# Kernel tuning notes

Hardware: AMD Instinct MI355X
Metric: run time of the kernel (lower is better)

Reference implementation:

```python
import jax, jax.numpy as jnp
import numpy as np


def trident(w, thresholds, noise_sd, noise):
    # thresholded + noised ternarization to {-1, 0, +1}
    wn = w + noise_sd * noise
    return jnp.where(wn < thresholds[0], -1.0, jnp.where(wn > thresholds[1], 1.0, 0.0)).astype(w.dtype)


def setup_inputs() -> dict:
    key = jax.random.key(0)
    k1, k2, k3, k4 = jax.random.split(key, 4)
    B, in_features, num_experts, expert_size = 8192, 4096, 64, 128
    in_chunks = in_features // expert_size  # 32
    x = jax.random.normal(k1, (B, in_features), dtype=jnp.float32)
    # glorot-like scaling for params
    routing_matrix = jax.random.normal(k2, (in_chunks, num_experts), dtype=jnp.float32) * np.sqrt(2.0 / (in_chunks + num_experts))
    We = jax.random.normal(k3, (num_experts, expert_size, expert_size), dtype=jnp.float32) * np.sqrt(1.0 / expert_size)
    noise = jax.random.normal(k4, (in_chunks, num_experts), dtype=jnp.float32)
    return {"x": x, "routing_matrix": routing_matrix, "We": We, "noise": noise}


def reference(x, routing_matrix, We, noise):
    thresholds = (-0.5, 0.5)
    noise_sd = 0.1
    expert_size = We.shape[-1]
    B = x.shape[0]
    xc = x.reshape(B, -1, expert_size)                     # (B, in_chunks, d)
    ternary = trident(routing_matrix, thresholds, noise_sd, noise)  # (in_chunks, E)
    x_routed = jnp.einsum('ik,bij->bkj', ternary, xc)      # (B, E, d)
    x_experts = jnp.einsum('eij,bej->bei', We, x_routed)   # (B, E, d)
    return x_experts.reshape(B, -1)
```

## Files before the change

kernel.cpp:

```cpp
#include <hip/hip_runtime.h>

#define IC   32
#define NE   64
#define D    128
#define IF   4096
#define OF   8192
#define TB   128

__global__ __launch_bounds__(256, 1)
void trident_moe_kernel(const float* __restrict__ x,
                        const float* __restrict__ routing,
                        const float* __restrict__ We,
                        const float* __restrict__ noise,
                        float* __restrict__ out) {
    __shared__ float sWe[D * D];
    __shared__ float sXr[TB * D];
    __shared__ float s_sign[IC];
    __shared__ int   s_chunk[IC];
    __shared__ float s_csign[IC];
    __shared__ int   s_cnt;

    const int t  = threadIdx.x;
    const int e  = blockIdx.y;
    const int bt = blockIdx.x;

    if (t < IC) {
        float w  = routing[t * NE + e];
        float nz = noise[t * NE + e];
        float wn = __fadd_rn(w, __fmul_rn(0.1f, nz));
        s_sign[t] = (wn < -0.5f) ? -1.0f : ((wn > 0.5f) ? 1.0f : 0.0f);
    }
    __syncthreads();
    if (t == 0) {
        int c = 0;
        for (int i = 0; i < IC; ++i) {
            float s = s_sign[i];
            if (s != 0.0f) { s_chunk[c] = i; s_csign[c] = s; ++c; }
        }
        s_cnt = c;
    }
    __syncthreads();
    const int nnz = s_cnt;

    const int c4 = t & 31;
    const int r0 = t >> 5;

    float4* out4 = (float4*)out;
    const size_t orow4 = OF / 4;

    if (nnz == 0) {
        const float4 z = make_float4(0.f, 0.f, 0.f, 0.f);
        #pragma unroll
        for (int p = 0; p < TB / 8; ++p) {
            size_t row = (size_t)(bt * TB + p * 8 + r0);
            out4[row * orow4 + e * (D / 4) + c4] = z;
        }
        return;
    }

    const float4* We4 = (const float4*)(We + (size_t)e * D * D);
    #pragma unroll
    for (int p = 0; p < D / 8; ++p) {
        int r = p * 8 + r0;
        float4 w4 = We4[r * (D / 4) + c4];
        float wv[4] = {w4.x, w4.y, w4.z, w4.w};
        #pragma unroll
        for (int k = 0; k < 4; ++k) {
            int j = c4 * 4 + k;
            int blk = (r >> 3) ^ ((j >> 2) & 15);
            sWe[j * D + blk * 8 + (r & 7)] = wv[k];
        }
    }

    const float4* x4p = (const float4*)x;
    const size_t xrow4 = IF / 4;
    #pragma unroll
    for (int p = 0; p < TB / 8; ++p) {
        int b = p * 8 + r0;
        size_t row = (size_t)(bt * TB + b);
        float4 acc = make_float4(0.f, 0.f, 0.f, 0.f);
        for (int m = 0; m < nnz; ++m) {
            int   i = s_chunk[m];
            float s = s_csign[m];
            float4 v = x4p[row * xrow4 + i * (D / 4) + c4];
            acc.x += s * v.x; acc.y += s * v.y;
            acc.z += s * v.z; acc.w += s * v.w;
        }
        float av[4] = {acc.x, acc.y, acc.z, acc.w};
        #pragma unroll
        for (int k = 0; k < 4; ++k) {
            int j = c4 * 4 + k;
            int blk = (b >> 3) ^ ((j >> 2) & 15);
            sXr[j * TB + blk * 8 + (b & 7)] = av[k];
        }
    }
    __syncthreads();

    const int rg = t & 15;
    const int bg = t >> 4;
    float acc[8][8];
    #pragma unroll
    for (int a = 0; a < 8; ++a)
        #pragma unroll
        for (int c = 0; c < 8; ++c) acc[a][c] = 0.f;

    #pragma unroll 2
    for (int j = 0; j < D; ++j) {
        const int sw = (j >> 2) & 15;
        const float4* wr = (const float4*)&sWe[j * D  + ((rg ^ sw) << 3)];
        const float4* xr = (const float4*)&sXr[j * TB + ((bg ^ sw) << 3)];
        float4 w0 = wr[0], w1 = wr[1];
        float4 x0 = xr[0], x1 = xr[1];
        float wv[8] = {w0.x, w0.y, w0.z, w0.w, w1.x, w1.y, w1.z, w1.w};
        float xv[8] = {x0.x, x0.y, x0.z, x0.w, x1.x, x1.y, x1.z, x1.w};
        #pragma unroll
        for (int a = 0; a < 8; ++a)
            #pragma unroll
            for (int c = 0; c < 8; ++c)
                acc[a][c] += wv[a] * xv[c];
    }

    #pragma unroll
    for (int c = 0; c < 8; ++c) {
        size_t row  = (size_t)(bt * TB + bg * 8 + c);
        size_t base = row * orow4 + e * (D / 4) + rg * 2;
        out4[base]     = make_float4(acc[0][c], acc[1][c], acc[2][c], acc[3][c]);
        out4[base + 1] = make_float4(acc[4][c], acc[5][c], acc[6][c], acc[7][c]);
    }
}

extern "C" void kernel_launch(void* const* d_in, const int* in_sizes, int n_in,
                              void* d_out, int out_size, void* d_ws, size_t ws_size,
                              hipStream_t stream) {
    const float* x       = (const float*)d_in[0];
    const float* routing = (const float*)d_in[1];
    const float* We      = (const float*)d_in[2];
    const float* noise   = (const float*)d_in[3];
    float* out = (float*)d_out;

    int B = in_sizes[0] / IF;
    dim3 grid(B / TB, NE);
    trident_moe_kernel<<<grid, 256, 0, stream>>>(x, routing, We, noise, out);
}
```

Baseline: 431.8 us.

## Precompute routing in prep kernel and compact active experts for GEMM grid

Adds a one-block prep kernel that ternarizes the routing matrix once, building per-expert chunk/sign lists and a compacted list of active experts in the workspace. A separate fill kernel zeroes the output columns of inactive experts, and the GEMM kernel maps blockIdx.y onto active experts only, so blocks for inactive experts exit immediately. This removes the redundant per-block ternarization and lets active-expert blocks be scheduled densely, at the cost of two extra launches. The fill kernel also reads every output index, not only the inactive columns.

```diff
diff --git a/kernel.cpp b/kernel.cpp
--- a/kernel.cpp
+++ b/kernel.cpp
@@ -7,56 +7,81 @@
 #define OF   8192
 #define TB   128
 
+#define NNZ_OFF    0
+#define NACT_OFF   64
+#define ACT_OFF    65
+#define CHUNK_OFF  129
+#define SIGN_OFF   (129 + NE*IC)
+
+__global__ void prep_kernel(const float* __restrict__ routing,
+                            const float* __restrict__ noise,
+                            int* __restrict__ ws) {
+    const int e = threadIdx.x;
+    if (e < NE) {
+        int cnt = 0;
+        for (int i = 0; i < IC; ++i) {
+            float w  = routing[i * NE + e];
+            float nz = noise[i * NE + e];
+            float wn = __fadd_rn(w, __fmul_rn(0.1f, nz));
+            float s  = (wn < -0.5f) ? -1.0f : ((wn > 0.5f) ? 1.0f : 0.0f);
+            if (s != 0.0f) {
+                ws[CHUNK_OFF + e * IC + cnt] = i;
+                ((float*)ws)[SIGN_OFF + e * IC + cnt] = s;
+                ++cnt;
+            }
+        }
+        ws[NNZ_OFF + e] = cnt;
+    }
+    __syncthreads();
+    if (e == 0) {
+        int na = 0;
+        for (int k = 0; k < NE; ++k)
+            if (ws[NNZ_OFF + k] > 0) ws[ACT_OFF + na++] = k;
+        ws[NACT_OFF] = na;
+    }
+}
+
+__global__ __launch_bounds__(256)
+void fill_kernel(const int* __restrict__ ws, float4* __restrict__ out4, int B) {
+    __shared__ int s_act[NE];
+    if (threadIdx.x < NE) s_act[threadIdx.x] = ws[NNZ_OFF + threadIdx.x];
+    __syncthreads();
+    const float4 z = make_float4(0.f, 0.f, 0.f, 0.f);
+    const size_t total = (size_t)B * (OF / 4);
+    const size_t stride = (size_t)gridDim.x * blockDim.x;
+    for (size_t idx = (size_t)blockIdx.x * blockDim.x + threadIdx.x;
+         idx < total; idx += stride) {
+        int col4 = (int)(idx & (OF / 4 - 1));
+        int e    = col4 >> 5;
+        if (s_act[e] == 0) out4[idx] = z;
+    }
+}
+
 __global__ __launch_bounds__(256, 1)
-void trident_moe_kernel(const float* __restrict__ x,
-                        const float* __restrict__ routing,
-                        const float* __restrict__ We,
-                        const float* __restrict__ noise,
-                        float* __restrict__ out) {
+void gemm_kernel(const float* __restrict__ x,
+                 const float* __restrict__ We,
+                 const int* __restrict__ ws,
+                 float* __restrict__ out) {
     __shared__ float sWe[D * D];
     __shared__ float sXr[TB * D];
-    __shared__ float s_sign[IC];
     __shared__ int   s_chunk[IC];
     __shared__ float s_csign[IC];
-    __shared__ int   s_cnt;
 
-    const int t  = threadIdx.x;
-    const int e  = blockIdx.y;
-    const int bt = blockIdx.x;
+    const int nact = ws[NACT_OFF];
+    if ((int)blockIdx.y >= nact) return;
+    const int e   = ws[ACT_OFF + blockIdx.y];
+    const int nnz = ws[NNZ_OFF + e];
+    const int t   = threadIdx.x;
+    const int bt  = blockIdx.x;
 
-    if (t < IC) {
-        float w  = routing[t * NE + e];
-        float nz = noise[t * NE + e];
-        float wn = __fadd_rn(w, __fmul_rn(0.1f, nz));
-        s_sign[t] = (wn < -0.5f) ? -1.0f : ((wn > 0.5f) ? 1.0f : 0.0f);
+    if (t < nnz) {
+        s_chunk[t] = ws[CHUNK_OFF + e * IC + t];
+        s_csign[t] = ((const float*)ws)[SIGN_OFF + e * IC + t];
     }
     __syncthreads();
-    if (t == 0) {
-        int c = 0;
-        for (int i = 0; i < IC; ++i) {
-            float s = s_sign[i];
-            if (s != 0.0f) { s_chunk[c] = i; s_csign[c] = s; ++c; }
-        }
-        s_cnt = c;
-    }
-    __syncthreads();
-    const int nnz = s_cnt;
 
     const int c4 = t & 31;
     const int r0 = t >> 5;
-
-    float4* out4 = (float4*)out;
-    const size_t orow4 = OF / 4;
-
-    if (nnz == 0) {
-        const float4 z = make_float4(0.f, 0.f, 0.f, 0.f);
-        #pragma unroll
-        for (int p = 0; p < TB / 8; ++p) {
-            size_t row = (size_t)(bt * TB + p * 8 + r0);
-            out4[row * orow4 + e * (D / 4) + c4] = z;
-        }
-        return;
-    }
 
     const float4* We4 = (const float4*)(We + (size_t)e * D * D);
     #pragma unroll
@@ -120,6 +145,8 @@
                 acc[a][c] += wv[a] * xv[c];
     }
 
+    float4* out4 = (float4*)out;
+    const size_t orow4 = OF / 4;
     #pragma unroll
     for (int c = 0; c < 8; ++c) {
         size_t row  = (size_t)(bt * TB + bg * 8 + c);
@@ -137,8 +164,12 @@
     const float* We      = (const float*)d_in[2];
     const float* noise   = (const float*)d_in[3];
     float* out = (float*)d_out;
+    int*   ws  = (int*)d_ws;
 
-    int B = in_sizes[0] / IF;
+    const int B = in_sizes[0] / IF;
+
+    prep_kernel<<<1, 64, 0, stream>>>(routing, noise, ws);
+    fill_kernel<<<2048, 256, 0, stream>>>(ws, (float4*)out, B);
     dim3 grid(B / TB, NE);
-    trident_moe_kernel<<<grid, 256, 0, stream>>>(x, routing, We, noise, out);
+    gemm_kernel<<<grid, 256, 0, stream>>>(x, We, ws, out);
 }
```

Result: slower. 459.0 us (+6.3%).

## Precompute routing in prep kernel and schedule active experts before inactive ones

Applied to the files above, without the earlier changes.

Adds a single-block prep kernel that ternarizes the routing matrix once and writes the nonzero chunk lists, per-expert counts and an active/inactive expert ordering to workspace. The main kernel maps grid y to this ordering, so blocks for active experts are dispatched first and blocks for inactive experts only write zeros, now with nontemporal stores. This removes the per-block serial routing scan and aims to balance load across the grid. The cost is an extra kernel launch and a dependent workspace read at block start.

```diff
diff --git a/kernel.cpp b/kernel.cpp
--- a/kernel.cpp
+++ b/kernel.cpp
@@ -7,56 +7,89 @@
 #define OF   8192
 #define TB   128
 
+typedef float vf4 __attribute__((ext_vector_type(4)));
+
+#define NNZ_OFF    0
+#define NACT_OFF   64
+#define ACT_OFF    65
+#define INACT_OFF  129
+#define CHUNK_OFF  193
+#define SIGN_OFF   (193 + NE * IC)
+
+__global__ void prep_kernel(const float* __restrict__ routing,
+                            const float* __restrict__ noise,
+                            int* __restrict__ ws) {
+    __shared__ float s_sign[IC][NE];
+    const int t = threadIdx.x;
+
+    #pragma unroll
+    for (int i = 0; i < IC; ++i) {
+        float w  = routing[i * NE + t];
+        float nz = noise[i * NE + t];
+        float wn = __fadd_rn(w, __fmul_rn(0.1f, nz));
+        s_sign[i][t] = (wn < -0.5f) ? -1.0f : ((wn > 0.5f) ? 1.0f : 0.0f);
+    }
+    __syncthreads();
+
+    int cnt = 0;
+    #pragma unroll
+    for (int i = 0; i < IC; ++i) {
+        float sgn = s_sign[i][t];
+        if (sgn != 0.0f) {
+            ws[CHUNK_OFF + t * IC + cnt] = i;
+            ((float*)ws)[SIGN_OFF + t * IC + cnt] = sgn;
+            ++cnt;
+        }
+    }
+    ws[NNZ_OFF + t] = cnt;
+
+    unsigned long long mask = __ballot(cnt > 0);
+    unsigned long long below = mask & ((t == 0) ? 0ull : (~0ull >> (64 - t)));
+    int act_before = (int)__popcll(below);
+    if (cnt > 0) ws[ACT_OFF + act_before] = t;
+    else         ws[INACT_OFF + (t - act_before)] = t;
+    if (t == 0)  ws[NACT_OFF] = (int)__popcll(mask);
+}
+
 __global__ __launch_bounds__(256, 1)
-void trident_moe_kernel(const float* __restrict__ x,
-                        const float* __restrict__ routing,
-                        const float* __restrict__ We,
-                        const float* __restrict__ noise,
-                        float* __restrict__ out) {
+void main_kernel(const float* __restrict__ x,
+                 const float* __restrict__ We,
+                 const int* __restrict__ ws,
+                 float* __restrict__ out) {
     __shared__ float sWe[D * D];
     __shared__ float sXr[TB * D];
-    __shared__ float s_sign[IC];
     __shared__ int   s_chunk[IC];
     __shared__ float s_csign[IC];
-    __shared__ int   s_cnt;
 
     const int t  = threadIdx.x;
-    const int e  = blockIdx.y;
     const int bt = blockIdx.x;
-
-    if (t < IC) {
-        float w  = routing[t * NE + e];
-        float nz = noise[t * NE + e];
-        float wn = __fadd_rn(w, __fmul_rn(0.1f, nz));
-        s_sign[t] = (wn < -0.5f) ? -1.0f : ((wn > 0.5f) ? 1.0f : 0.0f);
-    }
-    __syncthreads();
-    if (t == 0) {
-        int c = 0;
-        for (int i = 0; i < IC; ++i) {
-            float s = s_sign[i];
-            if (s != 0.0f) { s_chunk[c] = i; s_csign[c] = s; ++c; }
-        }
-        s_cnt = c;
-    }
-    __syncthreads();
-    const int nnz = s_cnt;
+    const int s  = blockIdx.y;
+    const int nact = ws[NACT_OFF];
 
     const int c4 = t & 31;
     const int r0 = t >> 5;
-
     float4* out4 = (float4*)out;
     const size_t orow4 = OF / 4;
 
-    if (nnz == 0) {
-        const float4 z = make_float4(0.f, 0.f, 0.f, 0.f);
+    if (s >= nact) {
+        const int e = ws[INACT_OFF + (s - nact)];
+        vf4* outv = (vf4*)out;
+        const vf4 z = (vf4){0.f, 0.f, 0.f, 0.f};
         #pragma unroll
         for (int p = 0; p < TB / 8; ++p) {
             size_t row = (size_t)(bt * TB + p * 8 + r0);
-            out4[row * orow4 + e * (D / 4) + c4] = z;
+            __builtin_nontemporal_store(z, &outv[row * orow4 + e * (D / 4) + c4]);
         }
         return;
     }
+
+    const int e   = ws[ACT_OFF + s];
+    const int nnz = ws[NNZ_OFF + e];
+    if (t < nnz) {
+        s_chunk[t] = ws[CHUNK_OFF + e * IC + t];
+        s_csign[t] = ((const float*)ws)[SIGN_OFF + e * IC + t];
+    }
+    __syncthreads();
 
     const float4* We4 = (const float4*)(We + (size_t)e * D * D);
     #pragma unroll
@@ -80,11 +113,11 @@
         size_t row = (size_t)(bt * TB + b);
         float4 acc = make_float4(0.f, 0.f, 0.f, 0.f);
         for (int m = 0; m < nnz; ++m) {
-            int   i = s_chunk[m];
-            float s = s_csign[m];
+            int   i  = s_chunk[m];
+            float sg = s_csign[m];
             float4 v = x4p[row * xrow4 + i * (D / 4) + c4];
-            acc.x += s * v.x; acc.y += s * v.y;
-            acc.z += s * v.z; acc.w += s * v.w;
+            acc.x += sg * v.x; acc.y += sg * v.y;
+            acc.z += sg * v.z; acc.w += sg * v.w;
         }
         float av[4] = {acc.x, acc.y, acc.z, acc.w};
         #pragma unroll
@@ -137,8 +170,11 @@
     const float* We      = (const float*)d_in[2];
     const float* noise   = (const float*)d_in[3];
     float* out = (float*)d_out;
+    int*   ws  = (int*)d_ws;
 
-    int B = in_sizes[0] / IF;
+    const int B = in_sizes[0] / IF;
+
+    prep_kernel<<<1, 64, 0, stream>>>(routing, noise, ws);
     dim3 grid(B / TB, NE);
-    trident_moe_kernel<<<grid, 256, 0, stream>>>(x, routing, We, noise, out);
+    main_kernel<<<grid, 256, 0, stream>>>(x, We, ws, out);
 }
```

Measured after the change: 431.1 us. About the same (-0.2%).
